# Kernel optimization log

Hardware: AMD Instinct MI355X
Metric: run time of the kernel (lower is better)

## Reference

```python
import math
import jax, jax.numpy as jnp
import numpy as np

N_KINDS = 8
D_MODEL = 256
B_FEAT = 24  # Fourier bands; MLP input dim is 2*B_FEAT
SIGMA = 8.0


def setup_inputs() -> dict:
    key = jax.random.key(0)
    ks = jax.random.split(key, 8)
    N, S = 32, 2048
    values = jax.random.normal(ks[0], (N, S, 1), dtype=jnp.float32)
    kinds = jax.random.randint(ks[1], (N, S), 0, N_KINDS, dtype=jnp.int32)
    # Frozen Fourier projection matrix (torch: randn(in_dim, B) * sigma, requires_grad=False)
    Bmat = jax.random.normal(ks[2], (1, B_FEAT), dtype=jnp.float32) * SIGMA
    # Kind embedding table
    kind_emb = jax.random.normal(ks[3], (N_KINDS, D_MODEL), dtype=jnp.float32) * 0.02
    # Per-kind two-layer MLP params
    W1 = jax.random.normal(ks[4], (N_KINDS, 2 * B_FEAT, D_MODEL), dtype=jnp.float32) / math.sqrt(2 * B_FEAT)
    b1 = jnp.zeros((N_KINDS, D_MODEL), dtype=jnp.float32)
    W2 = jax.random.normal(ks[5], (N_KINDS, D_MODEL, D_MODEL), dtype=jnp.float32) / math.sqrt(D_MODEL)
    b2 = jnp.zeros((N_KINDS, D_MODEL), dtype=jnp.float32)
    return {"values": values, "kinds": kinds, "Bmat": Bmat,
            "kind_emb": kind_emb, "W1": W1, "b1": b1, "W2": W2, "b2": b2}


def reference(values, kinds, Bmat, kind_emb, W1, b1, W2, b2):
    N, S, _ = values.shape
    T = N * S
    d = kind_emb.shape[-1]
    # Fourier features: [T, 2B]
    y = (2.0 * math.pi) * values.reshape(T, 1) @ Bmat  # [T, B]
    ff = jnp.concatenate([jnp.sin(y), jnp.cos(y)], axis=-1)  # [T, 2B]
    kinds_flat = kinds.reshape(T)
    out = jnp.zeros((T, d), dtype=values.dtype)
    # kinds partition the tokens, so masked combine == the torch scatter-assign
    for k in range(kind_emb.shape[0]):
        h = jax.nn.gelu(ff @ W1[k] + b1[k], approximate=False)  # torch GELU is exact erf
        o = h @ W2[k] + b2[k]  # [T, d]
        out = jnp.where((kinds_flat == k)[:, None], o, out)
    return out.reshape(N, S, d) + kind_emb[kinds]
```

## Files before the change

### kernel.cpp

```cpp
#include <hip/hip_runtime.h>
#include <hip/hip_bf16.h>
#include <math.h>


#define NK 8
#define DM 256
#define TMAX 65536
#define NBLK 256
#define W1PK 16384
#define W2PK 65536
#define LDSTRIDE 262

typedef __attribute__((ext_vector_type(8))) short   s16x8;
typedef __attribute__((ext_vector_type(8))) __bf16  bf16x8;
typedef __attribute__((ext_vector_type(4))) float   f32x4;
typedef __attribute__((ext_vector_type(2))) float   f32x2;
typedef __attribute__((ext_vector_type(4))) int     i32x4;

__device__ int   g_counts[NK];
__device__ __align__(16) int g_blkcnt[NBLK][NK];
__device__ int   g_bucket[(size_t)NK * TMAX];
__device__ __align__(16) short g_W1p[(size_t)NK * W1PK];
__device__ __align__(16) short g_W2p[(size_t)NK * W2PK];

static __device__ __forceinline__ short f2bf(float f) {
    __hip_bfloat16 h = __float2bfloat16(f);
    return __builtin_bit_cast(short, h);
}

static __device__ __forceinline__ short pkbf(float f) {
    unsigned u = __builtin_bit_cast(unsigned, f);
    return (short)((u + 0x8000u) >> 16);
}

static __device__ __forceinline__ f32x4 mfma16(s16x8 a, s16x8 b, f32x4 c) {
    return __builtin_amdgcn_mfma_f32_16x16x32_bf16(
        __builtin_bit_cast(bf16x8, a), __builtin_bit_cast(bf16x8, b), c, 0, 0, 0);
}

static __device__ __forceinline__ float gelu_fast(float x) {
    float t1 = x * x;
    float m  = fmaf(0.0713548162726f, t1, 1.59576912161f);
    float z  = m * x;
    float e  = __expf(-z);
    return x * __frcp_rn(1.0f + e);
}

__global__ __launch_bounds__(256) void prep_kernel(const float* __restrict__ W1,
                                                   const float* __restrict__ W2,
                                                   const int* __restrict__ kinds, int T) {
    __shared__ float ld[32 * LDSTRIDE];
    __shared__ int wcnt[4][NK];
    const int tid = threadIdx.x;
    const int bid = blockIdx.x;
    if (bid < 80) {
        const int isW1 = (bid >= 64);
        int kind, kt;
        if (isW1) { kind = (bid - 64) >> 1; kt = (bid - 64) & 1; }
        else      { kind = bid >> 3;        kt = bid & 7; }
        #pragma unroll
        for (int i = 0; i < 8; ++i) {
            int f = tid + i * 256;
            int row = f >> 6, col = (f & 63) * 4;
            int kk = kt * 32 + row;
            f32x4 v = (f32x4){0.f, 0.f, 0.f, 0.f};
            if (isW1) {
                if (kk < 48) v = *(const f32x4*)(W1 + ((size_t)kind * 48 + kk) * DM + col);
            } else {
                v = *(const f32x4*)(W2 + ((size_t)kind * DM + kk) * DM + col);
            }
            float* dst = &ld[row * LDSTRIDE + col];
            *(f32x2*)dst       = (f32x2){v[0], v[1]};
            *(f32x2*)(dst + 2) = (f32x2){v[2], v[3]};
        }
        __syncthreads();
        short* outp = isW1 ? (g_W1p + (size_t)kind * W1PK) : (g_W2p + (size_t)kind * W2PK);
        #pragma unroll
        for (int i = 0; i < 4; ++i) {
            int g = tid + i * 256;
            int ntile = g >> 6, l = g & 63;
            int kk0 = (l >> 4) * 8, n = ntile * 16 + (l & 15);
            s16x8 v;
            #pragma unroll
            for (int j = 0; j < 8; ++j) v[j] = f2bf(ld[(kk0 + j) * LDSTRIDE + n]);
            *(s16x8*)(outp + ((size_t)(kt * 16 + ntile) * 64 + l) * 8) = v;
        }
    } else {
        const int b = bid - 80;
        const int wave = tid >> 6, lane = tid & 63;
        int t = b * 256 + tid;
        int k = (t < T) ? kinds[t] : -1;
        #pragma unroll
        for (int kk = 0; kk < NK; ++kk) {
            unsigned long long m = __ballot(k == kk);
            if (lane == 0) wcnt[wave][kk] = __popcll(m);
        }
        __syncthreads();
        if (tid < NK) {
            int s = 0;
            #pragma unroll
            for (int w = 0; w < 4; ++w) s += wcnt[w][tid];
            g_blkcnt[b][tid] = s;
        }
    }
}

__global__ __launch_bounds__(256) void scatter_kernel(const int* __restrict__ kinds, int T) {
    __shared__ int cnt_s[NBLK * NK];
    __shared__ int chunksum[32][NK];
    __shared__ int chunkpref[32][NK];
    __shared__ int wcnt[4][NK];
    __shared__ int base_s[NK];
    const int tid = threadIdx.x, wave = tid >> 6, lane = tid & 63;
    const int b = blockIdx.x;
    {
        const i32x4* src = (const i32x4*)&g_blkcnt[0][0];
        i32x4* dst = (i32x4*)cnt_s;
        dst[tid]       = src[tid];
        dst[tid + 256] = src[tid + 256];
    }
    int t = b * 256 + tid;
    int k = (t < T) ? kinds[t] : -1;
    int rank = 0;
    #pragma unroll
    for (int kk = 0; kk < NK; ++kk) {
        unsigned long long m = __ballot(k == kk);
        if (lane == 0) wcnt[wave][kk] = __popcll(m);
        if (k == kk) rank = __popcll(m & ((1ull << lane) - 1ull));
    }
    __syncthreads();
    {
        int kk = tid & 7, ch = tid >> 3;
        int s = 0;
        #pragma unroll
        for (int i = 0; i < 8; ++i) s += cnt_s[(ch * 8 + i) * NK + kk];
        chunksum[ch][kk] = s;
    }
    __syncthreads();
    if (tid < NK) {
        int s = 0;
        #pragma unroll
        for (int ch = 0; ch < 32; ++ch) { chunkpref[ch][tid] = s; s += chunksum[ch][tid]; }
        if (b == 0) g_counts[tid] = s;
        int ch = b >> 3;
        int s2 = chunkpref[ch][tid];
        for (int bb = ch * 8; bb < b; ++bb) s2 += cnt_s[bb * NK + tid];
        base_s[tid] = s2;
        int ws = 0;
        #pragma unroll
        for (int w = 0; w < 4; ++w) { int c = wcnt[w][tid]; wcnt[w][tid] = ws; ws += c; }
    }
    __syncthreads();
    if (k >= 0)
        g_bucket[(size_t)k * T + base_s[k] + wcnt[wave][k] + rank] = t;
}

__global__ __launch_bounds__(256, 4) void fproj_gemm(
    const float* __restrict__ values, const float* __restrict__ Bmat,
    const float* __restrict__ kind_emb, const float* __restrict__ b1,
    const float* __restrict__ b2, float* __restrict__ out, int T)
{
    int cnts[NK];
    #pragma unroll
    for (int i = 0; i < NK; ++i) cnts[i] = g_counts[i];
    const int bid = blockIdx.x;
    int k = -1, m0 = 0, cum = 0, cnt = 0;
    #pragma unroll
    for (int kk = 0; kk < NK; ++kk) {
        int tk = (cnts[kk] + 31) >> 5;
        if (k < 0 && bid < cum + tk) { k = kk; m0 = (bid - cum) * 32; cnt = cnts[kk]; }
        cum += tk;
    }
    if (k < 0) return;
    const int valid = min(32, cnt - m0);
    const int* buck = g_bucket + (size_t)k * T + m0;

    __shared__ short Hpack[8192];

    const int tid  = threadIdx.x;
    const int wave = tid >> 6;
    const int lane = tid & 63;
    const int quad = lane >> 4;
    const int cl   = lane & 15;

    float vm[2];
    vm[0] = (cl < valid)      ? values[buck[cl]]      : 0.0f;
    vm[1] = (16 + cl < valid) ? values[buck[16 + cl]] : 0.0f;
    s16x8 a0[2], a1[2];
    #pragma unroll
    for (int mt = 0; mt < 2; ++mt) {
        float v = vm[mt];
        #pragma unroll
        for (int j = 0; j < 8; ++j) {
            int b0 = (quad == 3) ? j : quad * 8 + j;
            float r0 = __builtin_amdgcn_fractf(v * Bmat[b0]);
            float s0 = __builtin_amdgcn_sinf(r0);
            float c0 = __builtin_amdgcn_cosf(r0);
            a0[mt][j] = pkbf((quad == 3) ? c0 : s0);
            int b1i = min(8 * (quad + 1) + j, 23);
            float r1 = __builtin_amdgcn_fractf(v * Bmat[b1i]);
            float c1 = __builtin_amdgcn_cosf(r1);
            a1[mt][j] = pkbf((quad < 2) ? c1 : 0.0f);
        }
    }

    f32x4 acc[2][4];
    #pragma unroll
    for (int mt = 0; mt < 2; ++mt)
        #pragma unroll
        for (int nt = 0; nt < 4; ++nt) acc[mt][nt] = (f32x4){0.f, 0.f, 0.f, 0.f};
    const s16x8* B1p = (const s16x8*)(g_W1p + (size_t)k * W1PK);
    #pragma unroll
    for (int kt = 0; kt < 2; ++kt) {
        s16x8 bf[4];
        #pragma unroll
        for (int nt = 0; nt < 4; ++nt) bf[nt] = B1p[(kt * 16 + wave * 4 + nt) * 64 + lane];
        #pragma unroll
        for (int mt = 0; mt < 2; ++mt) {
            s16x8 a = kt ? a1[mt] : a0[mt];
            #pragma unroll
            for (int nt = 0; nt < 4; ++nt) acc[mt][nt] = mfma16(a, bf[nt], acc[mt][nt]);
        }
    }

    #pragma unroll
    for (int nt = 0; nt < 4; ++nt) {
        int c = wave * 64 + nt * 16 + cl;
        float bias = b1[k * DM + c];
        int kt2 = c >> 5, q2 = (c >> 3) & 3, j2 = c & 7;
        #pragma unroll
        for (int mt = 0; mt < 2; ++mt) {
            short* hp = Hpack + (kt2 * 2 + mt) * 512 + (q2 << 4) * 8 + j2;
            #pragma unroll
            for (int r = 0; r < 4; ++r) {
                int m = quad * 4 + r;
                float h = gelu_fast(acc[mt][nt][r] + bias);
                hp[m * 8] = pkbf(h);
            }
        }
    }
    __syncthreads();

    float addc[4];
    #pragma unroll
    for (int nt = 0; nt < 4; ++nt) {
        int c = wave * 64 + nt * 16 + cl;
        addc[nt] = b2[k * DM + c] + kind_emb[k * DM + c];
    }

    f32x4 acc2[2][4];
    #pragma unroll
    for (int mt = 0; mt < 2; ++mt)
        #pragma unroll
        for (int nt = 0; nt < 4; ++nt) acc2[mt][nt] = (f32x4){0.f, 0.f, 0.f, 0.f};
    const s16x8* Hp  = (const s16x8*)Hpack;
    const s16x8* B2p = (const s16x8*)(g_W2p + (size_t)k * W2PK);
    #pragma unroll
    for (int kt = 0; kt < 8; ++kt) {
        s16x8 am[2];
        #pragma unroll
        for (int mt = 0; mt < 2; ++mt) am[mt] = Hp[(kt * 2 + mt) * 64 + lane];
        s16x8 bf[4];
        #pragma unroll
        for (int nt = 0; nt < 4; ++nt) bf[nt] = B2p[(kt * 16 + wave * 4 + nt) * 64 + lane];
        #pragma unroll
        for (int mt = 0; mt < 2; ++mt)
            #pragma unroll
            for (int nt = 0; nt < 4; ++nt) acc2[mt][nt] = mfma16(am[mt], bf[nt], acc2[mt][nt]);
    }

    #pragma unroll
    for (int mt = 0; mt < 2; ++mt)
        #pragma unroll
        for (int r = 0; r < 4; ++r) {
            int row = mt * 16 + quad * 4 + r;
            if (row < valid) {
                size_t ro = (size_t)buck[row] * DM;
                #pragma unroll
                for (int nt = 0; nt < 4; ++nt) {
                    int c = wave * 64 + nt * 16 + cl;
                    __builtin_nontemporal_store(acc2[mt][nt][r] + addc[nt], out + ro + c);
                }
            }
        }
}

extern "C" void kernel_launch(void* const* d_in, const int* in_sizes, int n_in,
                              void* d_out, int out_size, void* d_ws, size_t ws_size,
                              hipStream_t stream) {
    const float* values   = (const float*)d_in[0];
    const int*   kinds    = (const int*)  d_in[1];
    const float* Bmat     = (const float*)d_in[2];
    const float* kind_emb = (const float*)d_in[3];
    const float* W1       = (const float*)d_in[4];
    const float* b1       = (const float*)d_in[5];
    const float* W2       = (const float*)d_in[6];
    const float* b2       = (const float*)d_in[7];
    float* out = (float*)d_out;
    const int T = in_sizes[0];

    prep_kernel<<<dim3(80 + NBLK), dim3(256), 0, stream>>>(W1, W2, kinds, T);
    scatter_kernel<<<dim3(NBLK), dim3(256), 0, stream>>>(kinds, T);
    fproj_gemm<<<dim3(T / 32 + NK), dim3(256), 0, stream>>>(values, Bmat, kind_emb,
                                                            b1, b2, out, T);
}
```

Baseline: 116.3 us.

## Make GEMM kernel persistent per kind with register-resident weights

Launches a fixed grid of 64 blocks per kind. Each block loads its kind's W1/W2 MFMA fragments into registers once and loops over 32-token tiles, with a double-buffered LDS hidden tile so one barrier per tile suffices. This removes the repeated per-tile weight loads from L2. Cosine features are computed as sine with a quarter-period phase shift. The cost is high register pressure (occupancy bound lowered to 2), fewer blocks in flight, and possible load imbalance if kind counts are skewed.

```diff
diff --git a/kernel.cpp b/kernel.cpp
--- a/kernel.cpp
+++ b/kernel.cpp
@@ -155,27 +155,15 @@
         g_bucket[(size_t)k * T + base_s[k] + wcnt[wave][k] + rank] = t;
 }
 
-__global__ __launch_bounds__(256, 4) void fproj_gemm(
+__global__ __launch_bounds__(256, 2) void fproj_gemm(
     const float* __restrict__ values, const float* __restrict__ Bmat,
     const float* __restrict__ kind_emb, const float* __restrict__ b1,
     const float* __restrict__ b2, float* __restrict__ out, int T)
 {
-    int cnts[NK];
-    #pragma unroll
-    for (int i = 0; i < NK; ++i) cnts[i] = g_counts[i];
-    const int bid = blockIdx.x;
-    int k = -1, m0 = 0, cum = 0, cnt = 0;
-    #pragma unroll
-    for (int kk = 0; kk < NK; ++kk) {
-        int tk = (cnts[kk] + 31) >> 5;
-        if (k < 0 && bid < cum + tk) { k = kk; m0 = (bid - cum) * 32; cnt = cnts[kk]; }
-        cum += tk;
-    }
-    if (k < 0) return;
-    const int valid = min(32, cnt - m0);
-    const int* buck = g_bucket + (size_t)k * T + m0;
-
-    __shared__ short Hpack[8192];
+    const int k    = blockIdx.x >> 6;
+    const int slot = blockIdx.x & 63;
+    const int cnt  = g_counts[k];
+    const int ntiles = (cnt + 31) >> 5;
 
     const int tid  = threadIdx.x;
     const int wave = tid >> 6;
@@ -183,106 +171,127 @@
     const int quad = lane >> 4;
     const int cl   = lane & 15;
 
-    float vm[2];
-    vm[0] = (cl < valid)      ? values[buck[cl]]      : 0.0f;
-    vm[1] = (16 + cl < valid) ? values[buck[16 + cl]] : 0.0f;
-    s16x8 a0[2], a1[2];
+    __shared__ short Hbuf[2][8192];
+
+    const s16x8* B1p = (const s16x8*)(g_W1p + (size_t)k * W1PK);
+    const s16x8* B2p = (const s16x8*)(g_W2p + (size_t)k * W2PK);
+    s16x8 w1f[2][4], w2f[8][4];
     #pragma unroll
-    for (int mt = 0; mt < 2; ++mt) {
-        float v = vm[mt];
-        #pragma unroll
-        for (int j = 0; j < 8; ++j) {
-            int b0 = (quad == 3) ? j : quad * 8 + j;
-            float r0 = __builtin_amdgcn_fractf(v * Bmat[b0]);
-            float s0 = __builtin_amdgcn_sinf(r0);
-            float c0 = __builtin_amdgcn_cosf(r0);
-            a0[mt][j] = pkbf((quad == 3) ? c0 : s0);
-            int b1i = min(8 * (quad + 1) + j, 23);
-            float r1 = __builtin_amdgcn_fractf(v * Bmat[b1i]);
-            float c1 = __builtin_amdgcn_cosf(r1);
-            a1[mt][j] = pkbf((quad < 2) ? c1 : 0.0f);
-        }
-    }
-
-    f32x4 acc[2][4];
+    for (int kt = 0; kt < 2; ++kt)
+        #pragma unroll
+        for (int nt = 0; nt < 4; ++nt) w1f[kt][nt] = B1p[(kt * 16 + wave * 4 + nt) * 64 + lane];
     #pragma unroll
-    for (int mt = 0; mt < 2; ++mt)
-        #pragma unroll
-        for (int nt = 0; nt < 4; ++nt) acc[mt][nt] = (f32x4){0.f, 0.f, 0.f, 0.f};
-    const s16x8* B1p = (const s16x8*)(g_W1p + (size_t)k * W1PK);
-    #pragma unroll
-    for (int kt = 0; kt < 2; ++kt) {
-        s16x8 bf[4];
-        #pragma unroll
-        for (int nt = 0; nt < 4; ++nt) bf[nt] = B1p[(kt * 16 + wave * 4 + nt) * 64 + lane];
-        #pragma unroll
-        for (int mt = 0; mt < 2; ++mt) {
-            s16x8 a = kt ? a1[mt] : a0[mt];
-            #pragma unroll
-            for (int nt = 0; nt < 4; ++nt) acc[mt][nt] = mfma16(a, bf[nt], acc[mt][nt]);
-        }
-    }
-
+    for (int kt = 0; kt < 8; ++kt)
+        #pragma unroll
+        for (int nt = 0; nt < 4; ++nt) w2f[kt][nt] = B2p[(kt * 16 + wave * 4 + nt) * 64 + lane];
+
+    float biasc[4], addc[4];
     #pragma unroll
     for (int nt = 0; nt < 4; ++nt) {
         int c = wave * 64 + nt * 16 + cl;
-        float bias = b1[k * DM + c];
-        int kt2 = c >> 5, q2 = (c >> 3) & 3, j2 = c & 7;
+        biasc[nt] = b1[k * DM + c];
+        addc[nt]  = b2[k * DM + c] + kind_emb[k * DM + c];
+    }
+
+    const int* buckbase = g_bucket + (size_t)k * T;
+
+    for (int tile = slot; tile < ntiles; tile += 64) {
+        const int m0    = tile * 32;
+        const int valid = min(32, cnt - m0);
+        const int* buck = buckbase + m0;
+        short* Hp = Hbuf[(tile >> 6) & 1];
+
+        float vm[2];
+        vm[0] = (cl < valid)      ? values[buck[cl]]      : 0.0f;
+        vm[1] = (16 + cl < valid) ? values[buck[16 + cl]] : 0.0f;
+        s16x8 a0[2], a1[2];
         #pragma unroll
         for (int mt = 0; mt < 2; ++mt) {
-            short* hp = Hpack + (kt2 * 2 + mt) * 512 + (q2 << 4) * 8 + j2;
-            #pragma unroll
-            for (int r = 0; r < 4; ++r) {
-                int m = quad * 4 + r;
-                float h = gelu_fast(acc[mt][nt][r] + bias);
-                hp[m * 8] = pkbf(h);
+            float v = vm[mt];
+            #pragma unroll
+            for (int j = 0; j < 8; ++j) {
+                int  b0   = (quad == 3) ? j : quad * 8 + j;
+                float ph0 = fmaf(v, Bmat[b0], (quad == 3) ? 0.25f : 0.0f);
+                a0[mt][j] = pkbf(__builtin_amdgcn_sinf(__builtin_amdgcn_fractf(ph0)));
+                int  b1i  = min(8 * (quad + 1) + j, 23);
+                float ph1 = fmaf(v, Bmat[b1i], 0.25f);
+                float c1  = __builtin_amdgcn_sinf(__builtin_amdgcn_fractf(ph1));
+                a1[mt][j] = pkbf((quad < 2) ? c1 : 0.0f);
             }
         }
-    }
-    __syncthreads();
-
-    float addc[4];
-    #pragma unroll
-    for (int nt = 0; nt < 4; ++nt) {
-        int c = wave * 64 + nt * 16 + cl;
-        addc[nt] = b2[k * DM + c] + kind_emb[k * DM + c];
-    }
-
-    f32x4 acc2[2][4];
-    #pragma unroll
-    for (int mt = 0; mt < 2; ++mt)
-        #pragma unroll
-        for (int nt = 0; nt < 4; ++nt) acc2[mt][nt] = (f32x4){0.f, 0.f, 0.f, 0.f};
-    const s16x8* Hp  = (const s16x8*)Hpack;
-    const s16x8* B2p = (const s16x8*)(g_W2p + (size_t)k * W2PK);
-    #pragma unroll
-    for (int kt = 0; kt < 8; ++kt) {
-        s16x8 am[2];
-        #pragma unroll
-        for (int mt = 0; mt < 2; ++mt) am[mt] = Hp[(kt * 2 + mt) * 64 + lane];
-        s16x8 bf[4];
-        #pragma unroll
-        for (int nt = 0; nt < 4; ++nt) bf[nt] = B2p[(kt * 16 + wave * 4 + nt) * 64 + lane];
-        #pragma unroll
-        for (int mt = 0; mt < 2; ++mt)
-            #pragma unroll
-            for (int nt = 0; nt < 4; ++nt) acc2[mt][nt] = mfma16(am[mt], bf[nt], acc2[mt][nt]);
-    }
-
-    #pragma unroll
-    for (int mt = 0; mt < 2; ++mt)
-        #pragma unroll
-        for (int r = 0; r < 4; ++r) {
-            int row = mt * 16 + quad * 4 + r;
-            if (row < valid) {
-                size_t ro = (size_t)buck[row] * DM;
-                #pragma unroll
-                for (int nt = 0; nt < 4; ++nt) {
-                    int c = wave * 64 + nt * 16 + cl;
-                    __builtin_nontemporal_store(acc2[mt][nt][r] + addc[nt], out + ro + c);
+
+        #pragma unroll
+        for (int np = 0; np < 2; ++np) {
+            f32x4 acc[2][2];
+            #pragma unroll
+            for (int mt = 0; mt < 2; ++mt)
+                #pragma unroll
+                for (int n2 = 0; n2 < 2; ++n2) acc[mt][n2] = (f32x4){0.f, 0.f, 0.f, 0.f};
+            #pragma unroll
+            for (int kt = 0; kt < 2; ++kt)
+                #pragma unroll
+                for (int mt = 0; mt < 2; ++mt) {
+                    s16x8 a = kt ? a1[mt] : a0[mt];
+                    #pragma unroll
+                    for (int n2 = 0; n2 < 2; ++n2)
+                        acc[mt][n2] = mfma16(a, w1f[kt][np * 2 + n2], acc[mt][n2]);
+                }
+            #pragma unroll
+            for (int n2 = 0; n2 < 2; ++n2) {
+                int nt = np * 2 + n2;
+                int c  = wave * 64 + nt * 16 + cl;
+                int kt2 = c >> 5, q2 = (c >> 3) & 3, j2 = c & 7;
+                #pragma unroll
+                for (int mt = 0; mt < 2; ++mt) {
+                    short* hp = Hp + (kt2 * 2 + mt) * 512 + (q2 << 4) * 8 + j2;
+                    #pragma unroll
+                    for (int r = 0; r < 4; ++r) {
+                        int m = quad * 4 + r;
+                        float h = gelu_fast(acc[mt][n2][r] + biasc[nt]);
+                        hp[m * 8] = pkbf(h);
+                    }
                 }
             }
         }
+        __syncthreads();
+
+        const s16x8* Hpv = (const s16x8*)Hp;
+        #pragma unroll
+        for (int np = 0; np < 2; ++np) {
+            f32x4 acc2[2][2];
+            #pragma unroll
+            for (int mt = 0; mt < 2; ++mt)
+                #pragma unroll
+                for (int n2 = 0; n2 < 2; ++n2) acc2[mt][n2] = (f32x4){0.f, 0.f, 0.f, 0.f};
+            #pragma unroll
+            for (int kt = 0; kt < 8; ++kt) {
+                s16x8 am[2];
+                #pragma unroll
+                for (int mt = 0; mt < 2; ++mt) am[mt] = Hpv[(kt * 2 + mt) * 64 + lane];
+                #pragma unroll
+                for (int mt = 0; mt < 2; ++mt)
+                    #pragma unroll
+                    for (int n2 = 0; n2 < 2; ++n2)
+                        acc2[mt][n2] = mfma16(am[mt], w2f[kt][np * 2 + n2], acc2[mt][n2]);
+            }
+            #pragma unroll
+            for (int mt = 0; mt < 2; ++mt)
+                #pragma unroll
+                for (int r = 0; r < 4; ++r) {
+                    int row = mt * 16 + quad * 4 + r;
+                    if (row < valid) {
+                        size_t ro = (size_t)buck[row] * DM;
+                        #pragma unroll
+                        for (int n2 = 0; n2 < 2; ++n2) {
+                            int nt = np * 2 + n2;
+                            int c  = wave * 64 + nt * 16 + cl;
+                            __builtin_nontemporal_store(acc2[mt][n2][r] + addc[nt],
+                                                        out + ro + c);
+                        }
+                    }
+                }
+        }
+    }
 }
 
 extern "C" void kernel_launch(void* const* d_in, const int* in_sizes, int n_in,
@@ -301,6 +310,6 @@
 
     prep_kernel<<<dim3(80 + NBLK), dim3(256), 0, stream>>>(W1, W2, kinds, T);
     scatter_kernel<<<dim3(NBLK), dim3(256), 0, stream>>>(kinds, T);
-    fproj_gemm<<<dim3(T / 32 + NK), dim3(256), 0, stream>>>(values, Bmat, kind_emb,
-                                                            b1, b2, out, T);
-}
+    fproj_gemm<<<dim3(NK * 64), dim3(256), 0, stream>>>(values, Bmat, kind_emb,
+                                                        b1, b2, out, T);
+}
```

Result: slower. 139.5 us (+20.0%).
